# Kernel tuning notes

Measured on AMD Instinct MI355X. Metric: run time of the kernel, lower is better.

## Reference

```python
import jax, jax.numpy as jnp
import numpy as np

N = 50000      # nodes
DEG = 32       # avg degree
E = N * DEG + N  # edges incl. self loops
IN_DIM = 512
H = 4          # heads
D = 128        # hidden per head
SLOPE = 0.2


def setup_inputs() -> dict:
    key = jax.random.key(0)
    ks = jax.random.split(key, 12)
    features = jax.random.normal(ks[0], (N, IN_DIM), dtype=jnp.float32)
    src_r = jax.random.randint(ks[1], (N * DEG,), 0, N)
    dst_r = jax.random.randint(ks[2], (N * DEG,), 0, N)
    loop = jnp.arange(N)
    src = jnp.concatenate([src_r, loop]).astype(jnp.int32)
    dst = jnp.concatenate([dst_r, loop]).astype(jnp.int32)
    ids = jax.random.randint(ks[3], (16,), 0, N)
    s0 = 1.0 / np.sqrt(IN_DIM)
    s1 = 1.0 / np.sqrt(H * D)
    fc_w0 = jax.random.normal(ks[4], (IN_DIM, H * D), dtype=jnp.float32) * s0
    attn_l0 = jax.random.normal(ks[5], (H, D), dtype=jnp.float32) * s1
    attn_r0 = jax.random.normal(ks[6], (H, D), dtype=jnp.float32) * s1
    bias0 = jnp.zeros((H * D,), dtype=jnp.float32)
    fc_w1 = jax.random.normal(ks[7], (H * D, H * D), dtype=jnp.float32) * s1
    attn_l1 = jax.random.normal(ks[8], (H, D), dtype=jnp.float32) * s1
    attn_r1 = jax.random.normal(ks[9], (H, D), dtype=jnp.float32) * s1
    bias1 = jnp.zeros((H * D,), dtype=jnp.float32)
    return dict(features=features, fc_w0=fc_w0, attn_l0=attn_l0, attn_r0=attn_r0,
                bias0=bias0, fc_w1=fc_w1, attn_l1=attn_l1, attn_r1=attn_r1,
                bias1=bias1, src=src, dst=dst, ids=ids)


def gat_layer(h, fc_w, attn_l, attn_r, bias, src, dst, residual):
    ft = (h @ fc_w).reshape(N, H, D)                     # [N,H,D]
    el = jnp.sum(ft * attn_l, axis=-1)                   # [N,H]
    er = jnp.sum(ft * attn_r, axis=-1)                   # [N,H]
    e = jax.nn.leaky_relu(el[src] + er[dst], SLOPE)      # [E,H]
    # edge softmax over incoming edges of each dst node (self-loops guarantee coverage)
    emax = jax.ops.segment_max(e, dst, num_segments=N)   # [N,H]
    ee = jnp.exp(e - emax[dst])
    esum = jax.ops.segment_sum(ee, dst, num_segments=N)  # [N,H]
    alpha = ee / esum[dst]                               # [E,H]
    out = jax.ops.segment_sum(alpha[:, :, None] * ft[src], dst, num_segments=N)  # [N,H,D]
    if residual:
        out = out + h.reshape(N, H, D)                   # res_fc is Identity (in == H*D)
    out = out + bias.reshape(1, H, D)
    out = jax.nn.elu(out)
    return out.reshape(N, H * D)


def reference(features, fc_w0, attn_l0, attn_r0, bias0, fc_w1, attn_l1, attn_r1,
              bias1, src, dst, ids):
    h = gat_layer(features, fc_w0, attn_l0, attn_r0, bias0, src, dst, residual=False)
    h = gat_layer(h, fc_w1, attn_l1, attn_r1, bias1, src, dst, residual=True)
    h = jnp.tanh(h)
    return h[ids]  # [B, H*D] gather per id2node lookup
```

## Files before the change

### kernel.cpp

```cpp
#include <hip/hip_runtime.h>
#include <hip/hip_bf16.h>

typedef short bf16x8 __attribute__((ext_vector_type(8)));
typedef float f32x4 __attribute__((ext_vector_type(4)));

#define HD 512
#define KDIM 512
#define NHEAD 4
#define DHEAD 128
#define C1CAP 1024
#define C2CAP 16384
#define E1CAP 2048
#define E2CAP 32768
#define SCATB 64

struct PassSM {
    unsigned bm[1568];
    int2 eBuf[256];
    int fBuf[256];
    int sid[16];
    int eCnt, fCnt, eBase, fBase, s_c;
};

union PrepSM {
    PassSM pass;
    float tile[64][65];
    int s_c;
};

struct GemmSM {
    __hip_bfloat16 As[128][40];
    __hip_bfloat16 Bs[128][40];
    float pel[2][128];
    float perr[2][128];
};

__device__ int detect_bf16(const unsigned short* f, int* s_c) {
    int c = 0;
#pragma unroll
    for (int k = 0; k < 4; ++k) {
        unsigned short u = f[2 * (threadIdx.x + k * 256)];
        int e = (u >> 7) & 0xFF;
        c += (e >= 96 && e <= 140) ? 1 : 0;
    }
#pragma unroll
    for (int off = 32; off; off >>= 1) c += __shfl_xor(c, off, 64);
    if (threadIdx.x == 0) *s_c = 0;
    __syncthreads();
    if ((threadIdx.x & 63) == 0) atomicAdd(s_c, c);
    __syncthreads();
    int r = (*s_c > 512) ? 1 : 0;
    __syncthreads();
    return r;
}

template<int MODE>
__device__ void pass_scan(int pid, const int* __restrict__ src,
                          const int* __restrict__ dst, int E, int B,
                          const int* __restrict__ map1g, PassSM& sm,
                          int2* __restrict__ elist, int* ecnt, int ecap,
                          int* __restrict__ cntArr,
                          int* __restrict__ mapm, int* __restrict__ Flist,
                          int* nFr, int fcap) {
    const int t = threadIdx.x;
    const int nq = E >> 2;
    const int gid = pid * 256 + t;
    if (gid < nq) {
        const int4 d4 = ((const int4*)dst)[gid];
        const int dv[4] = {d4.x, d4.y, d4.z, d4.w};
#pragma unroll
        for (int k = 0; k < 4; ++k) {
            const int d = dv[k];
            if ((sm.bm[d >> 5] >> (d & 31)) & 1u) {
                const int e = 4 * gid + k;
                int slot;
                if (MODE == 0) {
                    slot = 0;
                    for (int q = 0; q < B; ++q) if (sm.sid[q] == d) slot = q;
                } else {
                    slot = map1g[d]; if (slot < 0) slot = 0;
                }
                int p = atomicAdd(&cntArr[slot], 1);
                int2 v; v.x = src[e]; v.y = slot | (p << (MODE == 0 ? 4 : 10));
                int pp = atomicAdd(&sm.eCnt, 1);
                if (pp < 256) sm.eBuf[pp] = v;
                else { int q = atomicAdd(ecnt, 1); if (q < ecap) elist[q] = v; }
                const int s = v.x;
                if (atomicCAS(&mapm[s], -1, -2) == -1) {
                    int q = atomicAdd(&sm.fCnt, 1);
                    if (q < 256) sm.fBuf[q] = s;
                    else {
                        int g2 = atomicAdd(nFr, 1);
                        if (g2 < fcap) { Flist[g2] = s; mapm[s] = g2; }
                        else mapm[s] = 0;
                    }
                }
            }
        }
    }
    __syncthreads();
    const int ne = (sm.eCnt < 256) ? sm.eCnt : 256;
    const int nf = (sm.fCnt < 256) ? sm.fCnt : 256;
    if (t == 0 && ne) sm.eBase = atomicAdd(ecnt, ne);
    if (t == 64 && nf) sm.fBase = atomicAdd(nFr, nf);
    __syncthreads();
    for (int i = t; i < ne; i += 256) {
        int pos = sm.eBase + i;
        if (pos < ecap) elist[pos] = sm.eBuf[i];
    }
    for (int i = t; i < nf; i += 256) {
        int q = sm.fBase + i; int s = sm.fBuf[i];
        if (q < fcap) { Flist[q] = s; mapm[s] = q; }
        else mapm[s] = 0;
    }
}

__device__ void gemm_tile(const __hip_bfloat16* __restrict__ A,
                          const __hip_bfloat16* __restrict__ Bt,
                          __hip_bfloat16* __restrict__ C,
                          const float* __restrict__ al_, const float* __restrict__ ar_,
                          float* __restrict__ el, float* __restrict__ er,
                          int cntv, int m0, int n0, GemmSM& sm) {
    const int t = threadIdx.x;
    const int lane = t & 63, wave = t >> 6;
    const int wm = (wave >> 1) * 64, wn = (wave & 1) * 64;
    const int fr = lane & 15, fk = (lane >> 4) * 8;
    const int r0 = t >> 2;
    const int c0 = (t & 3) * 8;

    int arow[2];
#pragma unroll
    for (int r = 0; r < 2; ++r) {
        int rr = m0 + r * 64 + r0;
        if (rr >= cntv) rr = cntv - 1;
        arow[r] = rr;
    }

    auto loadAB = [&](int kt, uint4 va[2], uint4 vb[2]) {
#pragma unroll
        for (int r = 0; r < 2; ++r) {
            va[r] = *(const uint4*)&A[(size_t)arow[r] * KDIM + kt + c0];
            int row = r * 64 + r0;
            vb[r] = *(const uint4*)&Bt[(size_t)(n0 + row) * KDIM + kt + c0];
        }
    };

    f32x4 acc[4][4];
#pragma unroll
    for (int i = 0; i < 4; ++i)
#pragma unroll
        for (int j = 0; j < 4; ++j)
#pragma unroll
            for (int r = 0; r < 4; ++r) acc[i][j][r] = 0.f;

    auto stepStore = [&](uint4 va[2], uint4 vb[2]) {
#pragma unroll
        for (int r = 0; r < 2; ++r) {
            int row = r * 64 + r0;
            *(uint4*)&sm.As[row][c0] = va[r];
            *(uint4*)&sm.Bs[row][c0] = vb[r];
        }
        __syncthreads();
    };
    auto stepCompute = [&]() {
        bf16x8 af[4], bfr[4];
#pragma unroll
        for (int i = 0; i < 4; ++i) af[i]  = *(const bf16x8*)&sm.As[wm + i * 16 + fr][fk];
#pragma unroll
        for (int j = 0; j < 4; ++j) bfr[j] = *(const bf16x8*)&sm.Bs[wn + j * 16 + fr][fk];
#pragma unroll
        for (int i = 0; i < 4; ++i)
#pragma unroll
            for (int j = 0; j < 4; ++j)
                acc[i][j] = __builtin_amdgcn_mfma_f32_16x16x32_bf16(af[i], bfr[j], acc[i][j], 0, 0, 0);
        __syncthreads();
    };

    uint4 a0[2], b0[2], a1[2], b1[2];
    loadAB(0, a0, b0);
    loadAB(32, a1, b1);
    for (int kt = 0; kt < KDIM; kt += 64) {
        stepStore(a0, b0);
        if (kt + 64 < KDIM) loadAB(kt + 64, a0, b0);
        stepCompute();
        stepStore(a1, b1);
        if (kt + 96 < KDIM) loadAB(kt + 96, a1, b1);
        stepCompute();
    }

    const int cr = (lane >> 4) * 4;
    const int cc = lane & 15;
#pragma unroll
    for (int i = 0; i < 4; ++i)
#pragma unroll
        for (int j = 0; j < 4; ++j)
#pragma unroll
            for (int rg = 0; rg < 4; ++rg) {
                int m = m0 + wm + i * 16 + cr + rg;
                int n = n0 + wn + j * 16 + cc;
                C[(size_t)m * HD + n] = __float2bfloat16(acc[i][j][rg]);
            }

    const int h = n0 >> 7;
    float alv[4], arv[4];
#pragma unroll
    for (int j = 0; j < 4; ++j) {
        alv[j] = al_[h * DHEAD + wn + j * 16 + cc];
        arv[j] = ar_[h * DHEAD + wn + j * 16 + cc];
    }
#pragma unroll
    for (int i = 0; i < 4; ++i)
#pragma unroll
        for (int rg = 0; rg < 4; ++rg) {
            float sl = 0.f, sr = 0.f;
#pragma unroll
            for (int j = 0; j < 4; ++j) {
                float c = acc[i][j][rg];
                sl += c * alv[j];
                sr += c * arv[j];
            }
#pragma unroll
            for (int off = 1; off < 16; off <<= 1) {
                sl += __shfl_xor(sl, off, 16);
                sr += __shfl_xor(sr, off, 16);
            }
            if (cc == 0) {
                int row = wm + i * 16 + cr + rg;
                sm.pel[wn >> 6][row] = sl;
                sm.perr[wn >> 6][row] = sr;
            }
        }
    __syncthreads();
    if (t < 128) {
        int m = m0 + t;
        if (m < cntv) {
            el[m * NHEAD + h] = sm.pel[0][t] + sm.pel[1][t];
            er[m * NHEAD + h] = sm.perr[0][t] + sm.perr[1][t];
        }
    }
    __syncthreads();
}

__global__ __launch_bounds__(256) void prep_pass1_k(
    const void* __restrict__ features,
    const void* __restrict__ W0, const void* __restrict__ W1,
    __hip_bfloat16* __restrict__ Wt0, __hip_bfloat16* __restrict__ Wt1,
    const void* p0, const void* p1, const void* p2,
    const void* p3, const void* p4, const void* p5,
    float* __restrict__ smallc,
    const int* __restrict__ ids, int B, int* __restrict__ mapId,
    const int* __restrict__ src, const int* __restrict__ dst, int E,
    int2* __restrict__ E1l, int* __restrict__ counters,
    int* __restrict__ cnt1, int* __restrict__ map1, int* __restrict__ F1list) {
    __shared__ PrepSM sm;
    const int b = blockIdx.x;
    const int t = threadIdx.x;
    if (b < 128) {
        const int isbf = detect_bf16((const unsigned short*)features, &sm.s_c);
        const int mtx = b >> 6;
        const int tidx = b & 63;
        const int i0 = (tidx >> 3) * 64, j0 = (tidx & 7) * 64;
        const void* W = mtx ? W1 : W0;
        __hip_bfloat16* Wt = mtx ? Wt1 : Wt0;
        const int rr = t >> 6, cc = t & 63;
#pragma unroll
        for (int it = 0; it < 16; ++it) {
            int ii = rr + it * 4;
            size_t idx = (size_t)(i0 + ii) * 512 + j0 + cc;
            float v = isbf ? __bfloat162float(((const __hip_bfloat16*)W)[idx])
                           : ((const float*)W)[idx];
            sm.tile[ii][cc] = v;
        }
        __syncthreads();
#pragma unroll
        for (int it = 0; it < 16; ++it) {
            int jj = rr + it * 4;
            Wt[(size_t)(j0 + jj) * 512 + i0 + cc] = __float2bfloat16(sm.tile[cc][jj]);
        }
    } else if (b < 134) {
        const int isbf = detect_bf16((const unsigned short*)features, &sm.s_c);
        int which = b - 128;
        const void* p;
        switch (which) {
            case 0: p = p0; break;
            case 1: p = p1; break;
            case 2: p = p2; break;
            case 3: p = p3; break;
            case 4: p = p4; break;
            default: p = p5; break;
        }
#pragma unroll
        for (int r = 0; r < 2; ++r) {
            int e = t + r * 256;
            float v = isbf ? __bfloat162float(((const __hip_bfloat16*)p)[e])
                           : ((const float*)p)[e];
            smallc[which * 512 + e] = v;
        }
    } else if (b == 134) {
        if (t < B) atomicMax(&mapId[ids[t]], t);
    } else {
        const int pid = b - 135;
        for (int i = t; i < 1568; i += 256) sm.pass.bm[i] = 0u;
        if (t < 16) sm.pass.sid[t] = (t < B) ? ids[t] : -1;
        if (t == 0) { sm.pass.eCnt = 0; sm.pass.fCnt = 0; }
        __syncthreads();
        if (t < B) { int n = sm.pass.sid[t]; atomicOr(&sm.pass.bm[n >> 5], 1u << (n & 31)); }
        __syncthreads();
        pass_scan<0>(pid, src, dst, E, B, nullptr, sm.pass,
                     E1l, counters + 0, E1CAP, cnt1,
                     map1, F1list, counters + 2, C1CAP);
    }
}

__global__ __launch_bounds__(256) void pass2_k(
    const int* __restrict__ src, const int* __restrict__ dst, int E,
    const int* __restrict__ F1list, int* __restrict__ counters,
    const int* __restrict__ map1,
    int2* __restrict__ E2l, int* __restrict__ cnt2,
    int* __restrict__ map2, int* __restrict__ F2list) {
    __shared__ PassSM sm;
    const int t = threadIdx.x;
    for (int i = t; i < 1568; i += 256) sm.bm[i] = 0u;
    if (t == 0) { sm.eCnt = 0; sm.fCnt = 0; }
    __syncthreads();
    int nf1 = counters[2]; if (nf1 > C1CAP) nf1 = C1CAP;
    for (int i = t; i < nf1; i += 256) {
        int n = F1list[i];
        atomicOr(&sm.bm[n >> 5], 1u << (n & 31));
    }
    __syncthreads();
    pass_scan<1>(blockIdx.x, src, dst, E, 0, map1, sm,
                 E2l, counters + 1, E2CAP, cnt2,
                 map2, F2list, counters + 3, C2CAP);
}

__global__ __launch_bounds__(256) void gathscat_k(
    const void* __restrict__ feat, const int* __restrict__ F2list,
    const int* __restrict__ counters,
    const int* __restrict__ cnt1, const int* __restrict__ cnt2,
    const int2* __restrict__ E1l, const int2* __restrict__ E2l,
    const int* __restrict__ map1, const int* __restrict__ map2,
    int* __restrict__ off1, int* __restrict__ off2,
    int* __restrict__ b1, int* __restrict__ b2,
    __hip_bfloat16* __restrict__ Ac) {
    __shared__ int soff[1024];
    __shared__ int sc[256];
    __shared__ int s1[16];
    __shared__ int s_c;
    const int t = threadIdx.x;
    const int b = blockIdx.x;
    if (b < SCATB) {
        int c0 = cnt2[t * 4 + 0], c1 = cnt2[t * 4 + 1];
        int c2 = cnt2[t * 4 + 2], c3 = cnt2[t * 4 + 3];
        int tsum = c0 + c1 + c2 + c3;
        sc[t] = tsum;
        __syncthreads();
        for (int off = 1; off < 256; off <<= 1) {
            int x = (t >= off) ? sc[t - off] : 0;
            __syncthreads();
            sc[t] += x;
            __syncthreads();
        }
        int run = sc[t] - tsum;
        int b4 = t * 4;
        soff[b4 + 0] = run; run += c0;
        soff[b4 + 1] = run; run += c1;
        soff[b4 + 2] = run; run += c2;
        soff[b4 + 3] = run; run += c3;
        if (t == 0) {
            int acc = 0;
            for (int i = 0; i < 16; ++i) { s1[i] = acc; acc += cnt1[i]; }
            if (b == 0) {
                int a2 = 0;
                for (int i = 0; i < 16; ++i) { off1[i] = a2; a2 += cnt1[i]; }
                off1[16] = a2;
            }
        }
        if (b == 0) {
#pragma unroll
            for (int k = 0; k < 4; ++k) off2[b4 + k] = soff[b4 + k];
            if (t == 255) off2[1024] = run;
        }
        __syncthreads();
        int n2 = counters[1]; if (n2 > E2CAP) n2 = E2CAP;
        for (int i = b * 256 + t; i < n2; i += SCATB * 256) {
            int2 v = E2l[i];
            int y = v.y & 1023, p = v.y >> 10;
            int pos = soff[y] + p;
            int r = map2[v.x]; if (r < 0) r = 0;
            if (pos < E2CAP) b2[pos] = r;
        }
        int n1 = counters[0]; if (n1 > E1CAP) n1 = E1CAP;
        for (int i = b * 256 + t; i < n1; i += SCATB * 256) {
            int2 v = E1l[i];
            int y = v.y & 15, p = v.y >> 4;
            int pos = s1[y] + p;
            int r = map1[v.x]; if (r < 0) r = 0;
            if (pos < E1CAP) b1[pos] = r;
        }
    } else {
        const int isbf = detect_bf16((const unsigned short*)feat, &s_c);
        int cnt = counters[3]; if (cnt > C2CAP) cnt = C2CAP;
        for (int bb = b - SCATB; bb < cnt; bb += (int)gridDim.x - SCATB) {
            int row = F2list[bb];
            __hip_bfloat162 v;
            if (isbf) {
                v = *(const __hip_bfloat162*)&((const __hip_bfloat16*)feat)[(size_t)row * KDIM + t * 2];
            } else {
                const float2 f = *(const float2*)&((const float*)feat)[(size_t)row * KDIM + t * 2];
                v.x = __float2bfloat16(f.x);
                v.y = __float2bfloat16(f.y);
            }
            *(__hip_bfloat162*)&Ac[(size_t)bb * KDIM + t * 2] = v;
        }
    }
}

__global__ __launch_bounds__(256) void gemmel_k(
    const __hip_bfloat16* __restrict__ A,
    const __hip_bfloat16* __restrict__ Bt, __hip_bfloat16* __restrict__ C,
    const float* __restrict__ al_, const float* __restrict__ ar_,
    float* __restrict__ el, float* __restrict__ er,
    const int* __restrict__ countp, int cap) {
    __shared__ alignas(16) GemmSM sm;
    int cntv = *countp; if (cntv > cap) cntv = cap;
    const int nP = (cntv + 127) >> 7;
    const int xcd = blockIdx.x & 7;
    const int s = blockIdx.x >> 3;
    const int j = s & 3;
    const int perXcd = (int)gridDim.x >> 3;
    const int pstride = (perXcd >> 2) * 8;
    for (int p = (s >> 2) * 8 + xcd; p < nP; p += pstride)
        gemm_tile(A, Bt, C, al_, ar_, el, er, cntv, p * 128, j * 128, sm);
}

__global__ __launch_bounds__(256) void agg1_k(
    const int* __restrict__ off2, const int* __restrict__ b2,
    const int* __restrict__ F1list, const int* __restrict__ map2,
    const int* __restrict__ nF1p,
    const float* __restrict__ el, const float* __restrict__ er,
    const __hip_bfloat16* __restrict__ ftc,
    const float* __restrict__ bias,
    __hip_bfloat16* __restrict__ outc) {
    int b = blockIdx.x;
    if (b >= *nF1p) return;
    int n = F1list[b];
    const int h = threadIdx.x >> 6, lane = threadIdx.x & 63;
    int rn = map2[n]; if (rn < 0) rn = 0;
    float ern = er[rn * NHEAD + h];
    int beg = off2[b], end = off2[b + 1];
    float m = -3.0e38f, l = 0.f, a0 = 0.f, a1 = 0.f;
    int i = beg;
    for (; i + 8 <= end; i += 8) {
        int r8[8]; float ev[8]; __hip_bfloat162 fv[8];
#pragma unroll
        for (int k = 0; k < 8; ++k) {
            int r = b2[i + k]; if ((unsigned)r >= C2CAP) r = 0;
            r8[k] = r;
        }
#pragma unroll
        for (int k = 0; k < 8; ++k) {
            ev[k] = el[r8[k] * NHEAD + h];
            fv[k] = *(const __hip_bfloat162*)&ftc[(size_t)r8[k] * HD + h * DHEAD + lane * 2];
        }
#pragma unroll
        for (int k = 0; k < 8; ++k) {
            float e = ev[k] + ern;
            e = (e >= 0.f) ? e : 0.2f * e;
            float mn = fmaxf(m, e);
            float sc = __expf(m - mn);
            float w  = __expf(e - mn);
            l  = l * sc + w;
            a0 = a0 * sc + w * __bfloat162float(fv[k].x);
            a1 = a1 * sc + w * __bfloat162float(fv[k].y);
            m = mn;
        }
    }
    for (; i < end; ++i) {
        int r2 = b2[i]; if ((unsigned)r2 >= C2CAP) r2 = 0;
        float e = el[r2 * NHEAD + h] + ern;
        e = (e >= 0.f) ? e : 0.2f * e;
        float mn = fmaxf(m, e);
        float sc = __expf(m - mn);
        float w  = __expf(e - mn);
        const __hip_bfloat162 f = *(const __hip_bfloat162*)&ftc[(size_t)r2 * HD + h * DHEAD + lane * 2];
        l  = l * sc + w;
        a0 = a0 * sc + w * __bfloat162float(f.x);
        a1 = a1 * sc + w * __bfloat162float(f.y);
        m = mn;
    }
    float inv = (l > 0.f) ? 1.0f / l : 0.f;
    float o0 = a0 * inv, o1 = a1 * inv;
    const float2 bb = *(const float2*)&bias[h * DHEAD + lane * 2];
    o0 += bb.x; o1 += bb.y;
    o0 = (o0 > 0.f) ? o0 : expm1f(o0);
    o1 = (o1 > 0.f) ? o1 : expm1f(o1);
    __hip_bfloat162 o2;
    o2.x = __float2bfloat16(o0);
    o2.y = __float2bfloat16(o1);
    *(__hip_bfloat162*)&outc[(size_t)b * HD + h * DHEAD + lane * 2] = o2;
}

__global__ __launch_bounds__(256) void agg2_k(
    const int* __restrict__ off1, const int* __restrict__ b1,
    const int* __restrict__ ids, const int* __restrict__ mapId,
    const int* __restrict__ map1,
    const float* __restrict__ el, const float* __restrict__ er,
    const __hip_bfloat16* __restrict__ ftc,
    const __hip_bfloat16* __restrict__ resc,
    const float* __restrict__ bias,
    void* __restrict__ out, const void* __restrict__ features) {
    __shared__ int s_c;
    const int isbf = detect_bf16((const unsigned short*)features, &s_c);
    int b = blockIdx.x;
    int n = ids[b];
    int slot = mapId[n]; if (slot < 0) slot = 0;
    const int h = threadIdx.x >> 6, lane = threadIdx.x & 63;
    int rn = map1[n]; if (rn < 0) rn = 0;
    float ern = er[rn * NHEAD + h];
    int beg = off1[slot], end = off1[slot + 1];
    float m = -3.0e38f, l = 0.f, a0 = 0.f, a1 = 0.f;
    int i = beg;
    for (; i + 8 <= end; i += 8) {
        int r8[8]; float ev[8]; __hip_bfloat162 fv[8];
#pragma unroll
        for (int k = 0; k < 8; ++k) {
            int r = b1[i + k]; if ((unsigned)r >= C1CAP) r = 0;
            r8[k] = r;
        }
#pragma unroll
        for (int k = 0; k < 8; ++k) {
            ev[k] = el[r8[k] * NHEAD + h];
            fv[k] = *(const __hip_bfloat162*)&ftc[(size_t)r8[k] * HD + h * DHEAD + lane * 2];
        }
#pragma unroll
        for (int k = 0; k < 8; ++k) {
            float e = ev[k] + ern;
            e = (e >= 0.f) ? e : 0.2f * e;
            float mn = fmaxf(m, e);
            float sc = __expf(m - mn);
            float w  = __expf(e - mn);
            l  = l * sc + w;
            a0 = a0 * sc + w * __bfloat162float(fv[k].x);
            a1 = a1 * sc + w * __bfloat162float(fv[k].y);
            m = mn;
        }
    }
    for (; i < end; ++i) {
        int r1 = b1[i]; if ((unsigned)r1 >= C1CAP) r1 = 0;
        float e = el[r1 * NHEAD + h] + ern;
        e = (e >= 0.f) ? e : 0.2f * e;
        float mn = fmaxf(m, e);
        float sc = __expf(m - mn);
        float w  = __expf(e - mn);
        const __hip_bfloat162 f = *(const __hip_bfloat162*)&ftc[(size_t)r1 * HD + h * DHEAD + lane * 2];
        l  = l * sc + w;
        a0 = a0 * sc + w * __bfloat162float(f.x);
        a1 = a1 * sc + w * __bfloat162float(f.y);
        m = mn;
    }
    float inv = (l > 0.f) ? 1.0f / l : 0.f;
    float o0 = a0 * inv, o1 = a1 * inv;
    const __hip_bfloat162 rv = *(const __hip_bfloat162*)&resc[(size_t)rn * HD + h * DHEAD + lane * 2];
    o0 += __bfloat162float(rv.x);
    o1 += __bfloat162float(rv.y);
    const float2 bb = *(const float2*)&bias[h * DHEAD + lane * 2];
    o0 += bb.x; o1 += bb.y;
    o0 = (o0 > 0.f) ? o0 : expm1f(o0);
    o1 = (o1 > 0.f) ? o1 : expm1f(o1);
    o0 = tanhf(o0);
    o1 = tanhf(o1);
    size_t oi = (size_t)b * HD + h * DHEAD + lane * 2;
    if (isbf) {
        __hip_bfloat162 o2;
        o2.x = __float2bfloat16(o0);
        o2.y = __float2bfloat16(o1);
        *(__hip_bfloat162*)&((__hip_bfloat16*)out)[oi] = o2;
    } else {
        float2 o2; o2.x = o0; o2.y = o1;
        *(float2*)&((float*)out)[oi] = o2;
    }
}

extern "C" void kernel_launch(void* const* d_in, const int* in_sizes, int n_in,
                              void* d_out, int out_size, void* d_ws, size_t ws_size,
                              hipStream_t stream) {
    const void* features = d_in[0];
    const int* src = (const int*)d_in[9];
    const int* dst = (const int*)d_in[10];
    const int* ids = (const int*)d_in[11];

    const int N = in_sizes[0] / KDIM;
    const int E = in_sizes[9];
    const int B = in_sizes[11];

    char* w = (char*)d_ws;
    auto alloc = [&](size_t bytes) {
        void* p = (void*)w;
        w += (bytes + 255) & ~(size_t)255;
        return p;
    };
    __hip_bfloat16* Wt0 = (__hip_bfloat16*)alloc(512 * 512 * 2);
    __hip_bfloat16* Wt1 = (__hip_bfloat16*)alloc(512 * 512 * 2);
    float* smallc = (float*)alloc(6 * 512 * 4);
    int* maps  = (int*)alloc((size_t)3 * N * 4);
    int* mapId = maps;
    int* map1  = maps + N;
    int* map2  = maps + 2 * N;
    int2* E1l  = (int2*)alloc((size_t)E1CAP * 8);
    int2* E2l  = (int2*)alloc((size_t)E2CAP * 8);
    int* F1list = (int*)alloc(C1CAP * 4);
    int* F2list = (int*)alloc(C2CAP * 4);
    const int zwords = 8 + 16 + 1024;
    int* zmem = (int*)alloc((size_t)zwords * 4);
    int* counters = zmem;
    int* cnt1 = zmem + 8;
    int* cnt2 = cnt1 + 16;
    int* off1 = (int*)alloc(17 * 4);
    int* off2 = (int*)alloc(1025 * 4);
    int* b1   = (int*)alloc(E1CAP * 4);
    int* b2   = (int*)alloc(E2CAP * 4);
    __hip_bfloat16* Ac   = (__hip_bfloat16*)alloc((size_t)C2CAP * KDIM * 2);
    __hip_bfloat16* ft0c = (__hip_bfloat16*)alloc((size_t)C2CAP * HD * 2);
    float* el0 = (float*)alloc((size_t)C2CAP * NHEAD * 4);
    float* er0 = (float*)alloc((size_t)C2CAP * NHEAD * 4);
    __hip_bfloat16* h1c  = (__hip_bfloat16*)alloc((size_t)C1CAP * HD * 2);
    __hip_bfloat16* ft1c = (__hip_bfloat16*)alloc((size_t)C1CAP * HD * 2);
    float* el1 = (float*)alloc((size_t)C1CAP * NHEAD * 4);
    float* er1 = (float*)alloc((size_t)C1CAP * NHEAD * 4);

    hipMemsetAsync(maps, 0xFF, (size_t)3 * N * 4, stream);
    hipMemsetAsync(zmem, 0, (size_t)zwords * 4, stream);

    float* al0c = smallc + 0 * 512;
    float* ar0c = smallc + 1 * 512;
    float* b0c  = smallc + 2 * 512;
    float* al1c = smallc + 3 * 512;
    float* ar1c = smallc + 4 * 512;
    float* b1c  = smallc + 5 * 512;

    const int nblk_scan = (E / 4 + 255) / 256;

    prep_pass1_k<<<135 + nblk_scan, 256, 0, stream>>>(
        features, d_in[1], d_in[5], Wt0, Wt1,
        d_in[2], d_in[3], d_in[4], d_in[6], d_in[7], d_in[8],
        smallc, ids, B, mapId, src, dst, E,
        E1l, counters, cnt1, map1, F1list);

    pass2_k<<<nblk_scan, 256, 0, stream>>>(src, dst, E, F1list, counters, map1,
                                           E2l, cnt2, map2, F2list);

    gathscat_k<<<2048, 256, 0, stream>>>(features, F2list, counters, cnt1, cnt2,
                                         E1l, E2l, map1, map2,
                                         off1, off2, b1, b2, Ac);

    gemmel_k<<<512, 256, 0, stream>>>(Ac, Wt0, ft0c, al0c, ar0c, el0, er0,
                                      counters + 3, C2CAP);

    agg1_k<<<C1CAP, 256, 0, stream>>>(off2, b2, F1list, map2, counters + 2,
                                      el0, er0, ft0c, b0c, h1c);

    gemmel_k<<<32, 256, 0, stream>>>(h1c, Wt1, ft1c, al1c, ar1c, el1, er1,
                                     counters + 2, C1CAP);

    agg2_k<<<B, 256, 0, stream>>>(off1, b1, ids, mapId, map1,
                                  el1, er1, ft1c, h1c, b1c,
                                  d_out, features);
}
```

Baseline: 330.0 us.

## Fuse layer-2 GEMM and final aggregation into one kernel with spin-wait barrier

Merges the second GEMM and the final aggregation into one launch: 32 blocks run the GEMM tiles and bump a done counter, while the remaining blocks spin until it reaches 31 and then aggregate. It also collapses the two memsets into one by initialising the counters to -1 instead of 0, and adds +1 wherever a counter value is read. The aim is to remove one kernel launch and one memset. The spin-wait relies on the GEMM blocks being scheduled before or alongside the waiting blocks, and the -1 offset must be applied consistently everywhere a counter is read.

```diff
diff --git a/kernel.cpp b/kernel.cpp
--- a/kernel.cpp
+++ b/kernel.cpp
@@ -13,6 +13,7 @@
 #define E1CAP 2048
 #define E2CAP 32768
 #define SCATB 64
+
 
 struct PassSM {
     unsigned bm[1568];
@@ -80,17 +81,20 @@
                 } else {
                     slot = map1g[d]; if (slot < 0) slot = 0;
                 }
-                int p = atomicAdd(&cntArr[slot], 1);
+                int p = atomicAdd(&cntArr[slot], 1) + 1;
                 int2 v; v.x = src[e]; v.y = slot | (p << (MODE == 0 ? 4 : 10));
                 int pp = atomicAdd(&sm.eCnt, 1);
                 if (pp < 256) sm.eBuf[pp] = v;
-                else { int q = atomicAdd(ecnt, 1); if (q < ecap) elist[q] = v; }
+                else {
+                    int q = atomicAdd(ecnt, 1) + 1;
+                    if (q < ecap) elist[q] = v;
+                }
                 const int s = v.x;
                 if (atomicCAS(&mapm[s], -1, -2) == -1) {
                     int q = atomicAdd(&sm.fCnt, 1);
                     if (q < 256) sm.fBuf[q] = s;
                     else {
-                        int g2 = atomicAdd(nFr, 1);
+                        int g2 = atomicAdd(nFr, 1) + 1;
                         if (g2 < fcap) { Flist[g2] = s; mapm[s] = g2; }
                         else mapm[s] = 0;
                     }
@@ -101,8 +105,8 @@
     __syncthreads();
     const int ne = (sm.eCnt < 256) ? sm.eCnt : 256;
     const int nf = (sm.fCnt < 256) ? sm.fCnt : 256;
-    if (t == 0 && ne) sm.eBase = atomicAdd(ecnt, ne);
-    if (t == 64 && nf) sm.fBase = atomicAdd(nFr, nf);
+    if (t == 0 && ne) sm.eBase = atomicAdd(ecnt, ne) + 1;
+    if (t == 64 && nf) sm.fBase = atomicAdd(nFr, nf) + 1;
     __syncthreads();
     for (int i = t; i < ne; i += 256) {
         int pos = sm.eBase + i;
@@ -323,7 +327,7 @@
     for (int i = t; i < 1568; i += 256) sm.bm[i] = 0u;
     if (t == 0) { sm.eCnt = 0; sm.fCnt = 0; }
     __syncthreads();
-    int nf1 = counters[2]; if (nf1 > C1CAP) nf1 = C1CAP;
+    int nf1 = counters[2] + 1; if (nf1 > C1CAP) nf1 = C1CAP;
     for (int i = t; i < nf1; i += 256) {
         int n = F1list[i];
         atomicOr(&sm.bm[n >> 5], 1u << (n & 31));
@@ -350,8 +354,8 @@
     const int t = threadIdx.x;
     const int b = blockIdx.x;
     if (b < SCATB) {
-        int c0 = cnt2[t * 4 + 0], c1 = cnt2[t * 4 + 1];
-        int c2 = cnt2[t * 4 + 2], c3 = cnt2[t * 4 + 3];
+        int c0 = cnt2[t * 4 + 0] + 1, c1 = cnt2[t * 4 + 1] + 1;
+        int c2 = cnt2[t * 4 + 2] + 1, c3 = cnt2[t * 4 + 3] + 1;
         int tsum = c0 + c1 + c2 + c3;
         sc[t] = tsum;
         __syncthreads();
@@ -369,10 +373,10 @@
         soff[b4 + 3] = run; run += c3;
         if (t == 0) {
             int acc = 0;
-            for (int i = 0; i < 16; ++i) { s1[i] = acc; acc += cnt1[i]; }
+            for (int i = 0; i < 16; ++i) { s1[i] = acc; acc += cnt1[i] + 1; }
             if (b == 0) {
                 int a2 = 0;
-                for (int i = 0; i < 16; ++i) { off1[i] = a2; a2 += cnt1[i]; }
+                for (int i = 0; i < 16; ++i) { off1[i] = a2; a2 += cnt1[i] + 1; }
                 off1[16] = a2;
             }
         }
@@ -382,7 +386,7 @@
             if (t == 255) off2[1024] = run;
         }
         __syncthreads();
-        int n2 = counters[1]; if (n2 > E2CAP) n2 = E2CAP;
+        int n2 = counters[1] + 1; if (n2 > E2CAP) n2 = E2CAP;
         for (int i = b * 256 + t; i < n2; i += SCATB * 256) {
             int2 v = E2l[i];
             int y = v.y & 1023, p = v.y >> 10;
@@ -390,7 +394,7 @@
             int r = map2[v.x]; if (r < 0) r = 0;
             if (pos < E2CAP) b2[pos] = r;
         }
-        int n1 = counters[0]; if (n1 > E1CAP) n1 = E1CAP;
+        int n1 = counters[0] + 1; if (n1 > E1CAP) n1 = E1CAP;
         for (int i = b * 256 + t; i < n1; i += SCATB * 256) {
             int2 v = E1l[i];
             int y = v.y & 15, p = v.y >> 4;
@@ -400,7 +404,7 @@
         }
     } else {
         const int isbf = detect_bf16((const unsigned short*)feat, &s_c);
-        int cnt = counters[3]; if (cnt > C2CAP) cnt = C2CAP;
+        int cnt = counters[3] + 1; if (cnt > C2CAP) cnt = C2CAP;
         for (int bb = b - SCATB; bb < cnt; bb += (int)gridDim.x - SCATB) {
             int row = F2list[bb];
             __hip_bfloat162 v;
@@ -423,7 +427,7 @@
     float* __restrict__ el, float* __restrict__ er,
     const int* __restrict__ countp, int cap) {
     __shared__ alignas(16) GemmSM sm;
-    int cntv = *countp; if (cntv > cap) cntv = cap;
+    int cntv = *countp + 1; if (cntv > cap) cntv = cap;
     const int nP = (cntv + 127) >> 7;
     const int xcd = blockIdx.x & 7;
     const int s = blockIdx.x >> 3;
@@ -443,7 +447,7 @@
     const float* __restrict__ bias,
     __hip_bfloat16* __restrict__ outc) {
     int b = blockIdx.x;
-    if (b >= *nF1p) return;
+    if (b >= *nF1p + 1) return;
     int n = F1list[b];
     const int h = threadIdx.x >> 6, lane = threadIdx.x & 63;
     int rn = map2[n]; if (rn < 0) rn = 0;
@@ -501,21 +505,47 @@
     *(__hip_bfloat162*)&outc[(size_t)b * HD + h * DHEAD + lane * 2] = o2;
 }
 
-__global__ __launch_bounds__(256) void agg2_k(
+__global__ __launch_bounds__(256) void gemm2agg2_k(
+    const __hip_bfloat16* __restrict__ A,
+    const __hip_bfloat16* __restrict__ Bt,
+    __hip_bfloat16* __restrict__ C,
+    const float* __restrict__ al_, const float* __restrict__ ar_,
+    float* __restrict__ el, float* __restrict__ er,
+    const int* __restrict__ cnt1p,
+    int* __restrict__ done,
     const int* __restrict__ off1, const int* __restrict__ b1,
     const int* __restrict__ ids, const int* __restrict__ mapId,
     const int* __restrict__ map1,
-    const float* __restrict__ el, const float* __restrict__ er,
-    const __hip_bfloat16* __restrict__ ftc,
-    const __hip_bfloat16* __restrict__ resc,
     const float* __restrict__ bias,
     void* __restrict__ out, const void* __restrict__ features) {
-    __shared__ int s_c;
-    const int isbf = detect_bf16((const unsigned short*)features, &s_c);
-    int b = blockIdx.x;
+    __shared__ alignas(16) GemmSM sm;
+    const int t = threadIdx.x;
+    const int bid = blockIdx.x;
+    int cnt1v = *cnt1p + 1; if (cnt1v > C1CAP) cnt1v = C1CAP;
+    if (bid < 32) {
+        const int nP = (cnt1v + 127) >> 7;
+        const int xcd = bid & 7;
+        const int j = bid >> 3;
+        for (int p = xcd; p < nP; p += 8)
+            gemm_tile(A, Bt, C, al_, ar_, el, er, cnt1v, p * 128, j * 128, sm);
+        __syncthreads();
+        if (t == 0) {
+            __builtin_amdgcn_fence(__ATOMIC_RELEASE, "agent");
+            atomicAdd(done, 1);
+        }
+        return;
+    }
+    if (t == 0) {
+        while (__hip_atomic_load(done, __ATOMIC_RELAXED, __HIP_MEMORY_SCOPE_AGENT) < 31)
+            __builtin_amdgcn_s_sleep(8);
+        __builtin_amdgcn_fence(__ATOMIC_ACQUIRE, "agent");
+    }
+    __syncthreads();
+    const int isbf = detect_bf16((const unsigned short*)features, (int*)&sm);
+    const int b = bid - 32;
     int n = ids[b];
     int slot = mapId[n]; if (slot < 0) slot = 0;
-    const int h = threadIdx.x >> 6, lane = threadIdx.x & 63;
+    const int h = t >> 6, lane = t & 63;
     int rn = map1[n]; if (rn < 0) rn = 0;
     float ern = er[rn * NHEAD + h];
     int beg = off1[slot], end = off1[slot + 1];
@@ -531,7 +561,7 @@
 #pragma unroll
         for (int k = 0; k < 8; ++k) {
             ev[k] = el[r8[k] * NHEAD + h];
-            fv[k] = *(const __hip_bfloat162*)&ftc[(size_t)r8[k] * HD + h * DHEAD + lane * 2];
+            fv[k] = *(const __hip_bfloat162*)&C[(size_t)r8[k] * HD + h * DHEAD + lane * 2];
         }
 #pragma unroll
         for (int k = 0; k < 8; ++k) {
@@ -553,7 +583,7 @@
         float mn = fmaxf(m, e);
         float sc = __expf(m - mn);
         float w  = __expf(e - mn);
-        const __hip_bfloat162 f = *(const __hip_bfloat162*)&ftc[(size_t)r1 * HD + h * DHEAD + lane * 2];
+        const __hip_bfloat162 f = *(const __hip_bfloat162*)&C[(size_t)r1 * HD + h * DHEAD + lane * 2];
         l  = l * sc + w;
         a0 = a0 * sc + w * __bfloat162float(f.x);
         a1 = a1 * sc + w * __bfloat162float(f.y);
@@ -561,7 +591,7 @@
     }
     float inv = (l > 0.f) ? 1.0f / l : 0.f;
     float o0 = a0 * inv, o1 = a1 * inv;
-    const __hip_bfloat162 rv = *(const __hip_bfloat162*)&resc[(size_t)rn * HD + h * DHEAD + lane * 2];
+    const __hip_bfloat162 rv = *(const __hip_bfloat162*)&A[(size_t)rn * HD + h * DHEAD + lane * 2];
     o0 += __bfloat162float(rv.x);
     o1 += __bfloat162float(rv.y);
     const float2 bb = *(const float2*)&bias[h * DHEAD + lane * 2];
@@ -603,19 +633,20 @@
     __hip_bfloat16* Wt0 = (__hip_bfloat16*)alloc(512 * 512 * 2);
     __hip_bfloat16* Wt1 = (__hip_bfloat16*)alloc(512 * 512 * 2);
     float* smallc = (float*)alloc(6 * 512 * 4);
-    int* maps  = (int*)alloc((size_t)3 * N * 4);
+    const size_t mapsBytes = ((size_t)3 * N * 4 + 255) & ~(size_t)255;
+    int* maps = (int*)alloc((size_t)3 * N * 4);
+    const int zwords = 8 + 16 + 1024;
+    int* zmem = (int*)alloc((size_t)zwords * 4);
     int* mapId = maps;
     int* map1  = maps + N;
     int* map2  = maps + 2 * N;
+    int* counters = zmem;
+    int* cnt1 = zmem + 8;
+    int* cnt2 = cnt1 + 16;
     int2* E1l  = (int2*)alloc((size_t)E1CAP * 8);
     int2* E2l  = (int2*)alloc((size_t)E2CAP * 8);
     int* F1list = (int*)alloc(C1CAP * 4);
     int* F2list = (int*)alloc(C2CAP * 4);
-    const int zwords = 8 + 16 + 1024;
-    int* zmem = (int*)alloc((size_t)zwords * 4);
-    int* counters = zmem;
-    int* cnt1 = zmem + 8;
-    int* cnt2 = cnt1 + 16;
     int* off1 = (int*)alloc(17 * 4);
     int* off2 = (int*)alloc(1025 * 4);
     int* b1   = (int*)alloc(E1CAP * 4);
@@ -629,8 +660,7 @@
     float* el1 = (float*)alloc((size_t)C1CAP * NHEAD * 4);
     float* er1 = (float*)alloc((size_t)C1CAP * NHEAD * 4);
 
-    hipMemsetAsync(maps, 0xFF, (size_t)3 * N * 4, stream);
-    hipMemsetAsync(zmem, 0, (size_t)zwords * 4, stream);
+    hipMemsetAsync(maps, 0xFF, mapsBytes + (size_t)zwords * 4, stream);
 
     float* al0c = smallc + 0 * 512;
     float* ar0c = smallc + 1 * 512;
@@ -660,10 +690,8 @@
     agg1_k<<<C1CAP, 256, 0, stream>>>(off2, b2, F1list, map2, counters + 2,
                                       el0, er0, ft0c, b0c, h1c);
 
-    gemmel_k<<<32, 256, 0, stream>>>(h1c, Wt1, ft1c, al1c, ar1c, el1, er1,
-                                     counters + 2, C1CAP);
-
-    agg2_k<<<B, 256, 0, stream>>>(off1, b1, ids, mapId, map1,
-                                  el1, er1, ft1c, h1c, b1c,
-                                  d_out, features);
-}
+    gemm2agg2_k<<<32 + B, 256, 0, stream>>>(h1c, Wt1, ft1c, al1c, ar1c, el1, er1,
+                                            counters + 2, counters + 4,
+                                            off1, b1, ids, mapId, map1, b1c,
+                                            d_out, features);
+}
```

New measurement: 351.6 us. +6.5%, slower.
